# Kernel tuning notes

Hardware: AMD Instinct MI355X
Metric: run time of the kernel (lower is better)

## Reference

```python
import jax, jax.numpy as jnp
import numpy as np

D = 1024
B, T = 4, 2048


def _ln(x, g, b, eps=1e-5):
    mu = jnp.mean(x, axis=-1, keepdims=True)
    var = jnp.mean((x - mu) ** 2, axis=-1, keepdims=True)
    return (x - mu) * jax.lax.rsqrt(var + eps) * g + b


def setup_inputs() -> dict:
    key = jax.random.key(0)
    ks = jax.random.split(key, 24)
    s = 0.02
    lin = lambda k, o, i: jax.random.normal(k, (o, i), jnp.float32) * s
    return {
        "x": jax.random.normal(ks[0], (B, T, D), jnp.float32),
        "g1": jnp.ones((D,), jnp.float32),
        "be1": jnp.zeros((D,), jnp.float32),
        "w_lin1": lin(ks[1], D, D), "b_lin1": jnp.zeros((D,), jnp.float32),
        "wq": lin(ks[2], D, D), "bq": jnp.zeros((D,), jnp.float32),
        "wk": lin(ks[3], D, D), "bk": jnp.zeros((D,), jnp.float32),
        "wv": lin(ks[4], D, D), "bv": jnp.zeros((D,), jnp.float32),
        "w_lin2": lin(ks[5], D, D), "b_lin2": jnp.zeros((D,), jnp.float32),
        "g2": jnp.ones((D,), jnp.float32),
        "be2": jnp.zeros((D,), jnp.float32),
        "w_ff1": lin(ks[6], 2 * D, D), "b_ff1": jnp.zeros((2 * D,), jnp.float32),
        "w_ff2": lin(ks[7], D, 2 * D), "b_ff2": jnp.zeros((D,), jnp.float32),
    }


def reference(x, g1, be1, w_lin1, b_lin1, wq, bq, wk, bk, wv, bv,
              w_lin2, b_lin2, g2, be2, w_ff1, b_ff1, w_ff2, b_ff2):
    # x: [B,T,D]. Torch Linear: y = x @ W.T + b with W: [out,in]
    x = _ln(x, g1, be1)
    x = x @ w_lin1.T + b_lin1
    # single-head self-attention, scale = 1/sqrt(d_model) (matches source)
    q = x @ wq.T + bq
    k = x @ wk.T + bk
    v = x @ wv.T + bv
    scores = jnp.einsum('btd,bsd->bts', q, k) / jnp.sqrt(jnp.float32(x.shape[-1]))
    mask = jnp.tril(jnp.ones((x.shape[1], x.shape[1]), bool))  # [T,T]
    scores = jnp.where(mask, scores, -jnp.inf)
    probs = jax.nn.softmax(scores, axis=-1)
    attn = jnp.einsum('bts,bsd->btd', probs, v)
    x = x + (attn @ w_lin2.T + b_lin2)
    # FFN on norm2(x), exact (erf) GELU as torch default
    h = _ln(x, g2, be2)
    h = jax.nn.gelu(h @ w_ff1.T + b_ff1, approximate=False)
    x = x + (h @ w_ff2.T + b_ff2)
    return x
```

## Files before the change

kernel.cpp:

```cpp
#include <hip/hip_runtime.h>

typedef __attribute__((ext_vector_type(4))) float f32x4;
typedef __attribute__((ext_vector_type(8))) short short8;
typedef __attribute__((ext_vector_type(4))) unsigned short u16x4;
typedef __attribute__((ext_vector_type(8))) unsigned short u16x8;

#define MFMA(a, b, c) __builtin_amdgcn_mfma_f32_16x16x32_bf16(a, b, c, 0, 0, 0)
#define GLOAD16(g, l) __builtin_amdgcn_global_load_lds( \
    (const __attribute__((address_space(1))) unsigned int*)(g), \
    (__attribute__((address_space(3))) unsigned int*)(l), 16, 0, 0)

#define BARX() __builtin_amdgcn_s_barrier()
#define LGK0() asm volatile("s_waitcnt lgkmcnt(0)" ::: "memory")
#define VM6 asm volatile("s_waitcnt vmcnt(6)" ::: "memory")
#define VM0 asm volatile("s_waitcnt vmcnt(0)" ::: "memory")
#define NOWAIT ((void)0)

__device__ inline unsigned short f2bf(float f) {
    unsigned int u = __float_as_uint(f);
    u += 0x7fffu + ((u >> 16) & 1u);
    return (unsigned short)(u >> 16);
}

__global__ __launch_bounds__(256) void cvt_kernel(const float* __restrict__ in,
                                                  unsigned short* __restrict__ out, int n4) {
    int i = blockIdx.x * 256 + threadIdx.x;
    if (i < n4) {
        f32x4 v = *(const f32x4*)(in + (long long)i * 4);
        u16x4 o;
#pragma unroll
        for (int j = 0; j < 4; j++) o[j] = f2bf(v[j]);
        *(u16x4*)&out[(long long)i * 4] = o;
    }
}

__global__ __launch_bounds__(256) void ln_kernel(const float* __restrict__ x,
                                                 const float* __restrict__ g,
                                                 const float* __restrict__ be,
                                                 unsigned short* __restrict__ out) {
    const int row = blockIdx.x, tid = threadIdx.x;
    const float* px = x + (long long)row * 1024;
    f32x4 v = *(const f32x4*)(px + tid * 4);
    float s = v[0] + v[1] + v[2] + v[3];
    float q = v[0] * v[0] + v[1] * v[1] + v[2] * v[2] + v[3] * v[3];
#pragma unroll
    for (int o = 32; o; o >>= 1) { s += __shfl_xor(s, o); q += __shfl_xor(q, o); }
    __shared__ float sm[10];
    const int lane = tid & 63, wid = tid >> 6;
    if (lane == 0) { sm[wid] = s; sm[4 + wid] = q; }
    __syncthreads();
    if (tid == 0) {
        float ts = sm[0] + sm[1] + sm[2] + sm[3];
        float tq = sm[4] + sm[5] + sm[6] + sm[7];
        float mean = ts * (1.f / 1024.f);
        float var = tq * (1.f / 1024.f) - mean * mean;
        sm[8] = mean; sm[9] = rsqrtf(var + 1e-5f);
    }
    __syncthreads();
    float mean = sm[8], rs = sm[9];
    f32x4 gg = *(const f32x4*)(g + tid * 4);
    f32x4 bb = *(const f32x4*)(be + tid * 4);
    u16x4 o;
#pragma unroll
    for (int i = 0; i < 4; i++) o[i] = f2bf((v[i] - mean) * rs * gg[i] + bb[i]);
    *(u16x4*)&out[(long long)row * 1024 + tid * 4] = o;
}

__global__ __launch_bounds__(256) void softmax_kernel(float* __restrict__ S) {
    const int T = 2048;
    const int t = blockIdx.x, b = blockIdx.y, tid = threadIdx.x;
    float* row = S + ((long long)b * T + t) * T;
    const int base = tid * 8;
    f32x4 v0 = *(const f32x4*)(row + base);
    f32x4 v1 = *(const f32x4*)(row + base + 4);
    float mx = -1e30f;
#pragma unroll
    for (int i = 0; i < 4; i++) {
        if (base + i <= t)     mx = fmaxf(mx, v0[i]);
        if (base + 4 + i <= t) mx = fmaxf(mx, v1[i]);
    }
#pragma unroll
    for (int o = 32; o; o >>= 1) mx = fmaxf(mx, __shfl_xor(mx, o));
    __shared__ float sm[10];
    const int lane = tid & 63, wid = tid >> 6;
    if (lane == 0) sm[wid] = mx;
    __syncthreads();
    if (tid == 0) sm[8] = fmaxf(fmaxf(sm[0], sm[1]), fmaxf(sm[2], sm[3]));
    __syncthreads();
    float M = sm[8];
    float e[8]; float s = 0.f;
#pragma unroll
    for (int i = 0; i < 4; i++) {
        e[i]     = (base + i <= t)     ? __expf(v0[i] - M) : 0.f;
        e[4 + i] = (base + 4 + i <= t) ? __expf(v1[i] - M) : 0.f;
        s += e[i] + e[4 + i];
    }
#pragma unroll
    for (int o = 32; o; o >>= 1) s += __shfl_xor(s, o);
    if (lane == 0) sm[4 + wid] = s;
    __syncthreads();
    if (tid == 0) sm[9] = 1.f / (sm[4] + sm[5] + sm[6] + sm[7]);
    __syncthreads();
    float inv = sm[9];
    unsigned short* P = (unsigned short*)row;
    u16x8 o;
#pragma unroll
    for (int i = 0; i < 8; i++) o[i] = f2bf(e[i] * inv);
    *(u16x8*)&P[base] = o;
}

#define TILE(CB, PB, KPRE, PF, WAITER) do {                                         \
    const unsigned short* Lc = LDS + (CB) * 24576;                                  \
    unsigned short* Lp = LDS + (PB) * 24576;                                        \
    short8 Af0, Af1, Af2, Af3, Bf[4];                                               \
    Af0 = *(const short8*)(Lc + ao[0] + ks0);                                       \
    Af1 = *(const short8*)(Lc + ao[1] + ks0);                                       \
    _Pragma("unroll") for (int j = 0; j < 4; j++)                                   \
        Bf[j] = *(const short8*)(Lc + bo[j] + ks0);                                 \
    if (PF) { GLOAD16(srcA[0] + (KPRE), Lp + dstA[0]);                              \
              GLOAD16(srcA[1] + (KPRE), Lp + dstA[1]);                              \
              GLOAD16(srcA[2] + (KPRE), Lp + dstA[2]); }                            \
    BARX(); LGK0();                                                                 \
    __builtin_amdgcn_s_setprio(1);                                                  \
    _Pragma("unroll") for (int j = 0; j < 4; j++) {                                 \
        acc[0][j] = MFMA(Af0, Bf[j], acc[0][j]);                                    \
        acc[1][j] = MFMA(Af1, Bf[j], acc[1][j]); }                                  \
    __builtin_amdgcn_s_setprio(0); BARX();                                          \
    Af2 = *(const short8*)(Lc + ao[2] + ks0);                                       \
    Af3 = *(const short8*)(Lc + ao[3] + ks0);                                       \
    if (PF) { GLOAD16(srcA[3] + (KPRE), Lp + dstA[3]);                              \
              GLOAD16(srcB[0] + (KPRE), Lp + dstB[0]);                              \
              GLOAD16(srcB[1] + (KPRE), Lp + dstB[1]); }                            \
    BARX(); LGK0();                                                                 \
    __builtin_amdgcn_s_setprio(1);                                                  \
    _Pragma("unroll") for (int j = 0; j < 4; j++) {                                 \
        acc[2][j] = MFMA(Af2, Bf[j], acc[2][j]);                                    \
        acc[3][j] = MFMA(Af3, Bf[j], acc[3][j]); }                                  \
    __builtin_amdgcn_s_setprio(0); BARX();                                          \
    Af0 = *(const short8*)(Lc + ao[0] + ks1);                                       \
    Af1 = *(const short8*)(Lc + ao[1] + ks1);                                       \
    _Pragma("unroll") for (int j = 0; j < 4; j++)                                   \
        Bf[j] = *(const short8*)(Lc + bo[j] + ks1);                                 \
    BARX(); LGK0();                                                                 \
    __builtin_amdgcn_s_setprio(1);                                                  \
    _Pragma("unroll") for (int j = 0; j < 4; j++) {                                 \
        acc[0][j] = MFMA(Af0, Bf[j], acc[0][j]);                                    \
        acc[1][j] = MFMA(Af1, Bf[j], acc[1][j]); }                                  \
    __builtin_amdgcn_s_setprio(0); BARX();                                          \
    Af2 = *(const short8*)(Lc + ao[2] + ks1);                                       \
    Af3 = *(const short8*)(Lc + ao[3] + ks1);                                       \
    WAITER;                                                                         \
    BARX(); LGK0();                                                                 \
    __builtin_amdgcn_s_setprio(1);                                                  \
    _Pragma("unroll") for (int j = 0; j < 4; j++) {                                 \
        acc[2][j] = MFMA(Af2, Bf[j], acc[2][j]);                                    \
        acc[3][j] = MFMA(Af3, Bf[j], acc[3][j]); }                                  \
    __builtin_amdgcn_s_setprio(0); BARX();                                          \
} while (0)

template <int MODE>
__global__ __launch_bounds__(512, 2) void gemm_bt(
    const unsigned short* __restrict__ A, int lda, long long sA,
    const unsigned short* __restrict__ Bw, int ldb, long long sB,
    const float* __restrict__ bias,
    const float* __restrict__ resid, long long sR,
    float* __restrict__ outf, unsigned short* __restrict__ outb,
    int ldo, long long sO, int K, float scale, int flags) {
    const int m0 = blockIdx.y * 256, n0 = blockIdx.x * 128;
    if ((flags & 1) && n0 >= m0 + 256) return;
    const int bz = blockIdx.z;
    A += (long long)bz * sA; Bw += (long long)bz * sB;
    if (resid) resid += (long long)bz * sR;
    if (outf) outf += (long long)bz * sO;
    if (outb) outb += (long long)bz * sO;
    const int Keff = (flags & 2) ? (m0 + 256 < K ? m0 + 256 : K) : K;
    const int nt = Keff >> 6;

    __shared__ __align__(16) unsigned short LDS[3 * 24576];

    const int tid = threadIdx.x, lane = tid & 63, wid = tid >> 6;

    const unsigned short* srcA[4]; int dstA[4];
    const unsigned short* srcB[2]; int dstB[2];
#pragma unroll
    for (int g = 0; g < 4; g++) {
        int p = g * 512 + wid * 64 + lane;
        int r = p >> 3, cs = (p & 7) ^ (r & 7);
        srcA[g] = A + (long long)(m0 + r) * lda + cs * 8;
        dstA[g] = g * 4096 + wid * 512;
    }
#pragma unroll
    for (int g = 0; g < 2; g++) {
        int p = g * 512 + wid * 64 + lane;
        int r = p >> 3, cs = (p & 7) ^ (r & 7);
        srcB[g] = Bw + (long long)(n0 + r) * ldb + cs * 8;
        dstB[g] = 16384 + g * 4096 + wid * 512;
    }

    const int wm = (wid >> 1) * 64, wn = (wid & 1) * 64;
    const int fr = lane & 15;
    int ao[4], bo[4];
#pragma unroll
    for (int i = 0; i < 4; i++) ao[i] = (wm + i * 16 + fr) * 64;
#pragma unroll
    for (int j = 0; j < 4; j++) bo[j] = 16384 + (wn + j * 16 + fr) * 64;
    const int ks0 = (((lane >> 4)) ^ (fr & 7)) * 8;
    const int ks1 = ((4 + (lane >> 4)) ^ (fr & 7)) * 8;

    f32x4 acc[4][4] = {};

#pragma unroll
    for (int g = 0; g < 4; g++) GLOAD16(srcA[g], LDS + dstA[g]);
#pragma unroll
    for (int g = 0; g < 2; g++) GLOAD16(srcB[g], LDS + dstB[g]);
#pragma unroll
    for (int g = 0; g < 4; g++) GLOAD16(srcA[g] + 64, LDS + 24576 + dstA[g]);
#pragma unroll
    for (int g = 0; g < 2; g++) GLOAD16(srcB[g] + 64, LDS + 24576 + dstB[g]);
    VM6; BARX();
    __builtin_amdgcn_sched_barrier(0);

    int c = 0, p = 2, kpre = 128;
    for (int t = 0; t < nt - 2; ++t) {
        TILE(c, p, kpre, true, VM6);
        c = (c == 2) ? 0 : c + 1;
        p = (p == 2) ? 0 : p + 1;
        kpre += 64;
    }
    TILE(c, p, 0, false, VM0);
    c = (c == 2) ? 0 : c + 1;
    TILE(c, p, 0, false, NOWAIT);

    const int cc = lane & 15, rr = (lane >> 4) * 4;
#pragma unroll
    for (int fm = 0; fm < 4; fm++)
#pragma unroll
        for (int fn = 0; fn < 4; fn++) {
            f32x4 av = acc[fm][fn];
            int colg = n0 + wn + fn * 16 + cc;
            int rowg0 = m0 + wm + fm * 16 + rr;
            float bv = bias ? bias[colg] : 0.f;
            if (MODE == 3) {
                u16x4 o;
#pragma unroll
                for (int i = 0; i < 4; i++) o[i] = f2bf((av[i] + bv) * scale);
                *(u16x4*)&outb[(long long)colg * ldo + rowg0] = o;
            } else {
#pragma unroll
                for (int i = 0; i < 4; i++) {
                    float v = av[i] + bv;
                    long long idx = (long long)(rowg0 + i) * ldo + colg;
                    if (MODE == 0) outf[idx] = v;
                    if (MODE == 1) outf[idx] = v + resid[idx];
                    if (MODE == 2) outb[idx] = f2bf(v * scale);
                    if (MODE == 4) { outf[idx] = v; outb[idx] = f2bf(v); }
                    if (MODE == 5) outb[idx] = f2bf(0.5f * v * (1.f + erff(v * 0.70710678f)));
                }
            }
        }
}

extern "C" void kernel_launch(void* const* d_in, const int* in_sizes, int n_in,
                              void* d_out, int out_size, void* d_ws, size_t ws_size,
                              hipStream_t stream) {
    const float* x      = (const float*)d_in[0];
    const float* g1     = (const float*)d_in[1];
    const float* be1    = (const float*)d_in[2];
    const float* b_lin1 = (const float*)d_in[4];
    const float* bq     = (const float*)d_in[6];
    const float* bk     = (const float*)d_in[8];
    const float* bv     = (const float*)d_in[10];
    const float* b_lin2 = (const float*)d_in[12];
    const float* g2     = (const float*)d_in[13];
    const float* be2    = (const float*)d_in[14];
    const float* b_ff1  = (const float*)d_in[16];
    const float* b_ff2  = (const float*)d_in[18];

    const long long MB = 1024LL * 1024LL;
    char* ws = (char*)d_ws;
    unsigned short* xn1 = (unsigned short*)(ws + 0);
    unsigned short* x1b = (unsigned short*)(ws + 16 * MB);
    float*          S   = (float*)(ws + 0);
    float*          x1f = (float*)(ws + 64 * MB);
    unsigned short* xn2 = (unsigned short*)(ws + 64 * MB);
    unsigned short* qb  = (unsigned short*)(ws + 96 * MB);
    unsigned short* kb  = (unsigned short*)(ws + 112 * MB);
    unsigned short* vT  = (unsigned short*)(ws + 128 * MB);
    unsigned short* attn= (unsigned short*)(ws + 96 * MB);
    unsigned short* h   = (unsigned short*)(ws + 96 * MB);
    float*          x2  = (float*)(ws + 144 * MB);
    unsigned short* wb1 = (unsigned short*)(ws + 176 * MB);
    unsigned short* wbq = (unsigned short*)(ws + 178 * MB);
    unsigned short* wbk = (unsigned short*)(ws + 180 * MB);
    unsigned short* wbv = (unsigned short*)(ws + 182 * MB);
    unsigned short* wb2 = (unsigned short*)(ws + 184 * MB);
    unsigned short* wbf1= (unsigned short*)(ws + 186 * MB);
    unsigned short* wbf2= (unsigned short*)(ws + 190 * MB);

    auto cvt = [&](const void* src, unsigned short* dst, long long n) {
        int n4 = (int)(n / 4);
        cvt_kernel<<<(n4 + 255) / 256, 256, 0, stream>>>((const float*)src, dst, n4);
    };
    cvt(d_in[3], wb1, 1048576);
    cvt(d_in[5], wbq, 1048576);
    cvt(d_in[7], wbk, 1048576);
    cvt(d_in[9], wbv, 1048576);
    cvt(d_in[11], wb2, 1048576);
    cvt(d_in[15], wbf1, 2097152);
    cvt(d_in[17], wbf2, 2097152);

    ln_kernel<<<8192, 256, 0, stream>>>(x, g1, be1, xn1);
    gemm_bt<4><<<dim3(8, 32, 1), 512, 0, stream>>>(xn1, 1024, 0, wb1, 1024, 0, b_lin1,
        nullptr, 0, x1f, x1b, 1024, 0, 1024, 1.f, 0);
    gemm_bt<2><<<dim3(8, 32, 1), 512, 0, stream>>>(x1b, 1024, 0, wbq, 1024, 0, bq,
        nullptr, 0, nullptr, qb, 1024, 0, 1024, 0.03125f, 0);
    gemm_bt<2><<<dim3(8, 32, 1), 512, 0, stream>>>(x1b, 1024, 0, wbk, 1024, 0, bk,
        nullptr, 0, nullptr, kb, 1024, 0, 1024, 1.f, 0);
    gemm_bt<3><<<dim3(8, 8, 4), 512, 0, stream>>>(x1b, 1024, 2048LL * 1024, wbv, 1024, 0, bv,
        nullptr, 0, nullptr, vT, 2048, 2097152LL, 1024, 1.f, 0);
    gemm_bt<0><<<dim3(16, 8, 4), 512, 0, stream>>>(qb, 1024, 2097152LL, kb, 1024, 2097152LL,
        nullptr, nullptr, 0, S, nullptr, 2048, 4194304LL, 1024, 1.f, 1);
    softmax_kernel<<<dim3(2048, 4), 256, 0, stream>>>(S);
    gemm_bt<2><<<dim3(8, 8, 4), 512, 0, stream>>>((unsigned short*)S, 4096, 8388608LL,
        vT, 2048, 2097152LL, nullptr, nullptr, 0, nullptr, attn, 1024, 2097152LL, 2048, 1.f, 2);
    gemm_bt<1><<<dim3(8, 32, 1), 512, 0, stream>>>(attn, 1024, 0, wb2, 1024, 0, b_lin2,
        x1f, 0, x2, nullptr, 1024, 0, 1024, 1.f, 0);
    ln_kernel<<<8192, 256, 0, stream>>>(x2, g2, be2, xn2);
    gemm_bt<5><<<dim3(16, 32, 1), 512, 0, stream>>>(xn2, 1024, 0, wbf1, 1024, 0, b_ff1,
        nullptr, 0, nullptr, h, 2048, 0, 1024, 1.f, 0);
    gemm_bt<1><<<dim3(8, 32, 1), 512, 0, stream>>>(h, 2048, 0, wbf2, 2048, 0, b_ff2,
        x2, 0, (float*)d_out, nullptr, 1024, 0, 2048, 1.f, 0);
}
```

Baseline: 512.8 us.

## Add 256x256-tile GEMM, fuse Q/K projections, fold Q scale into weights

Adds a gemm_wide kernel with 256x256 output tiles and a K-step of 32 (8x4 fragments per wave), used for the fused QK projection, the QK^T scores and the FF1 GEMM. Q and K projections become one GEMM over contiguous wbq/wbk weights with a concatenated bias, and the 1/32 attention scale is folded into the Q weight conversion and bias. The existing tile macro is restructured to issue all four A fragments per MFMA group, halving barrier phases. Larger tiles cut global reloads and launches, but raise register pressure and leave fewer blocks for the grid.

```diff
diff --git a/kernel.cpp b/kernel.cpp
--- a/kernel.cpp
+++ b/kernel.cpp
@@ -13,6 +13,7 @@
 #define BARX() __builtin_amdgcn_s_barrier()
 #define LGK0() asm volatile("s_waitcnt lgkmcnt(0)" ::: "memory")
 #define VM6 asm volatile("s_waitcnt vmcnt(6)" ::: "memory")
+#define VM4 asm volatile("s_waitcnt vmcnt(4)" ::: "memory")
 #define VM0 asm volatile("s_waitcnt vmcnt(0)" ::: "memory")
 #define NOWAIT ((void)0)
 
@@ -23,15 +24,24 @@
 }
 
 __global__ __launch_bounds__(256) void cvt_kernel(const float* __restrict__ in,
-                                                  unsigned short* __restrict__ out, int n4) {
+                                                  unsigned short* __restrict__ out, int n4,
+                                                  float scale) {
     int i = blockIdx.x * 256 + threadIdx.x;
     if (i < n4) {
         f32x4 v = *(const f32x4*)(in + (long long)i * 4);
         u16x4 o;
 #pragma unroll
-        for (int j = 0; j < 4; j++) o[j] = f2bf(v[j]);
+        for (int j = 0; j < 4; j++) o[j] = f2bf(v[j] * scale);
         *(u16x4*)&out[(long long)i * 4] = o;
     }
+}
+
+__global__ __launch_bounds__(256) void biascat_kernel(const float* __restrict__ bq,
+                                                      const float* __restrict__ bk,
+                                                      float* __restrict__ out) {
+    int i = blockIdx.x * 256 + threadIdx.x;
+    if (i < 1024) out[i] = bq[i] * 0.03125f;
+    else if (i < 2048) out[i] = bk[i - 1024];
 }
 
 __global__ __launch_bounds__(256) void ln_kernel(const float* __restrict__ x,
@@ -109,12 +119,42 @@
     *(u16x8*)&P[base] = o;
 }
 
-#define TILE(CB, PB, KPRE, PF, WAITER) do {                                         \
+#define EPILOGUE(FM_COUNT) do {                                                     \
+    const int cc = lane & 15, rr = (lane >> 4) * 4;                                 \
+    _Pragma("unroll")                                                               \
+    for (int fm = 0; fm < FM_COUNT; fm++)                                           \
+        _Pragma("unroll")                                                           \
+        for (int fn = 0; fn < 4; fn++) {                                            \
+            f32x4 av = acc[fm][fn];                                                 \
+            int colg = n0 + wn + fn * 16 + cc;                                      \
+            int rowg0 = m0 + wm + fm * 16 + rr;                                     \
+            float bv = bias ? bias[colg] : 0.f;                                     \
+            if (MODE == 3) {                                                        \
+                u16x4 o;                                                            \
+                _Pragma("unroll")                                                   \
+                for (int i = 0; i < 4; i++) o[i] = f2bf((av[i] + bv) * scale);      \
+                *(u16x4*)&outb[(long long)colg * ldo + rowg0] = o;                  \
+            } else {                                                                \
+                _Pragma("unroll")                                                   \
+                for (int i = 0; i < 4; i++) {                                       \
+                    float v = av[i] + bv;                                           \
+                    long long idx = (long long)(rowg0 + i) * ldo + colg;            \
+                    if (MODE == 0) outf[idx] = v;                                   \
+                    if (MODE == 1) outf[idx] = v + resid[idx];                      \
+                    if (MODE == 2) outb[idx] = f2bf(v * scale);                     \
+                    if (MODE == 4) { outf[idx] = v; outb[idx] = f2bf(v); }          \
+                    if (MODE == 5) outb[idx] = f2bf(0.5f * v * (1.f + erff(v * 0.70710678f))); \
+                }                                                                   \
+            }                                                                       \
+        }                                                                           \
+} while (0)
+
+#define TILE_B(CB, PB, KPRE, PF, WAITER) do {                                       \
     const unsigned short* Lc = LDS + (CB) * 24576;                                  \
     unsigned short* Lp = LDS + (PB) * 24576;                                        \
-    short8 Af0, Af1, Af2, Af3, Bf[4];                                               \
-    Af0 = *(const short8*)(Lc + ao[0] + ks0);                                       \
-    Af1 = *(const short8*)(Lc + ao[1] + ks0);                                       \
+    short8 Af[4], Bf[4];                                                            \
+    _Pragma("unroll") for (int i = 0; i < 4; i++)                                   \
+        Af[i] = *(const short8*)(Lc + ao[i] + ks0);                                 \
     _Pragma("unroll") for (int j = 0; j < 4; j++)                                   \
         Bf[j] = *(const short8*)(Lc + bo[j] + ks0);                                 \
     if (PF) { GLOAD16(srcA[0] + (KPRE), Lp + dstA[0]);                              \
@@ -122,39 +162,23 @@
               GLOAD16(srcA[2] + (KPRE), Lp + dstA[2]); }                            \
     BARX(); LGK0();                                                                 \
     __builtin_amdgcn_s_setprio(1);                                                  \
-    _Pragma("unroll") for (int j = 0; j < 4; j++) {                                 \
-        acc[0][j] = MFMA(Af0, Bf[j], acc[0][j]);                                    \
-        acc[1][j] = MFMA(Af1, Bf[j], acc[1][j]); }                                  \
+    _Pragma("unroll") for (int i = 0; i < 4; i++)                                   \
+        _Pragma("unroll") for (int j = 0; j < 4; j++)                               \
+            acc[i][j] = MFMA(Af[i], Bf[j], acc[i][j]);                              \
     __builtin_amdgcn_s_setprio(0); BARX();                                          \
-    Af2 = *(const short8*)(Lc + ao[2] + ks0);                                       \
-    Af3 = *(const short8*)(Lc + ao[3] + ks0);                                       \
+    _Pragma("unroll") for (int i = 0; i < 4; i++)                                   \
+        Af[i] = *(const short8*)(Lc + ao[i] + ks1);                                 \
+    _Pragma("unroll") for (int j = 0; j < 4; j++)                                   \
+        Bf[j] = *(const short8*)(Lc + bo[j] + ks1);                                 \
     if (PF) { GLOAD16(srcA[3] + (KPRE), Lp + dstA[3]);                              \
               GLOAD16(srcB[0] + (KPRE), Lp + dstB[0]);                              \
               GLOAD16(srcB[1] + (KPRE), Lp + dstB[1]); }                            \
-    BARX(); LGK0();                                                                 \
-    __builtin_amdgcn_s_setprio(1);                                                  \
-    _Pragma("unroll") for (int j = 0; j < 4; j++) {                                 \
-        acc[2][j] = MFMA(Af2, Bf[j], acc[2][j]);                                    \
-        acc[3][j] = MFMA(Af3, Bf[j], acc[3][j]); }                                  \
-    __builtin_amdgcn_s_setprio(0); BARX();                                          \
-    Af0 = *(const short8*)(Lc + ao[0] + ks1);                                       \
-    Af1 = *(const short8*)(Lc + ao[1] + ks1);                                       \
-    _Pragma("unroll") for (int j = 0; j < 4; j++)                                   \
-        Bf[j] = *(const short8*)(Lc + bo[j] + ks1);                                 \
-    BARX(); LGK0();                                                                 \
-    __builtin_amdgcn_s_setprio(1);                                                  \
-    _Pragma("unroll") for (int j = 0; j < 4; j++) {                                 \
-        acc[0][j] = MFMA(Af0, Bf[j], acc[0][j]);                                    \
-        acc[1][j] = MFMA(Af1, Bf[j], acc[1][j]); }                                  \
-    __builtin_amdgcn_s_setprio(0); BARX();                                          \
-    Af2 = *(const short8*)(Lc + ao[2] + ks1);                                       \
-    Af3 = *(const short8*)(Lc + ao[3] + ks1);                                       \
     WAITER;                                                                         \
     BARX(); LGK0();                                                                 \
     __builtin_amdgcn_s_setprio(1);                                                  \
-    _Pragma("unroll") for (int j = 0; j < 4; j++) {                                 \
-        acc[2][j] = MFMA(Af2, Bf[j], acc[2][j]);                                    \
-        acc[3][j] = MFMA(Af3, Bf[j], acc[3][j]); }                                  \
+    _Pragma("unroll") for (int i = 0; i < 4; i++)                                   \
+        _Pragma("unroll") for (int j = 0; j < 4; j++)                               \
+            acc[i][j] = MFMA(Af[i], Bf[j], acc[i][j]);                              \
     __builtin_amdgcn_s_setprio(0); BARX();                                          \
 } while (0)
 
@@ -222,42 +246,112 @@
 
     int c = 0, p = 2, kpre = 128;
     for (int t = 0; t < nt - 2; ++t) {
-        TILE(c, p, kpre, true, VM6);
+        TILE_B(c, p, kpre, true, VM6);
         c = (c == 2) ? 0 : c + 1;
         p = (p == 2) ? 0 : p + 1;
         kpre += 64;
     }
-    TILE(c, p, 0, false, VM0);
+    TILE_B(c, p, 0, false, VM0);
     c = (c == 2) ? 0 : c + 1;
-    TILE(c, p, 0, false, NOWAIT);
-
-    const int cc = lane & 15, rr = (lane >> 4) * 4;
-#pragma unroll
-    for (int fm = 0; fm < 4; fm++)
-#pragma unroll
-        for (int fn = 0; fn < 4; fn++) {
-            f32x4 av = acc[fm][fn];
-            int colg = n0 + wn + fn * 16 + cc;
-            int rowg0 = m0 + wm + fm * 16 + rr;
-            float bv = bias ? bias[colg] : 0.f;
-            if (MODE == 3) {
-                u16x4 o;
-#pragma unroll
-                for (int i = 0; i < 4; i++) o[i] = f2bf((av[i] + bv) * scale);
-                *(u16x4*)&outb[(long long)colg * ldo + rowg0] = o;
-            } else {
-#pragma unroll
-                for (int i = 0; i < 4; i++) {
-                    float v = av[i] + bv;
-                    long long idx = (long long)(rowg0 + i) * ldo + colg;
-                    if (MODE == 0) outf[idx] = v;
-                    if (MODE == 1) outf[idx] = v + resid[idx];
-                    if (MODE == 2) outb[idx] = f2bf(v * scale);
-                    if (MODE == 4) { outf[idx] = v; outb[idx] = f2bf(v); }
-                    if (MODE == 5) outb[idx] = f2bf(0.5f * v * (1.f + erff(v * 0.70710678f)));
-                }
-            }
-        }
+    TILE_B(c, p, 0, false, NOWAIT);
+
+    EPILOGUE(4);
+}
+
+#define TILE_A(CB, PB, KPRE, PF, WAITER) do {                                       \
+    const unsigned short* Lc = LDS + (CB) * 16384;                                  \
+    unsigned short* Lp = LDS + (PB) * 16384;                                        \
+    short8 Af[4], Bf[4];                                                            \
+    _Pragma("unroll") for (int i = 0; i < 4; i++)                                   \
+        Af[i] = *(const short8*)(Lc + aoW[i] + ksW);                                \
+    _Pragma("unroll") for (int j = 0; j < 4; j++)                                   \
+        Bf[j] = *(const short8*)(Lc + boW[j] + ksW);                                \
+    if (PF) { GLOAD16(srcA[0] + (KPRE), Lp + dstA[0]);                              \
+              GLOAD16(srcB[0] + (KPRE), Lp + dstB[0]); }                            \
+    BARX(); LGK0();                                                                 \
+    __builtin_amdgcn_s_setprio(1);                                                  \
+    _Pragma("unroll") for (int i = 0; i < 4; i++)                                   \
+        _Pragma("unroll") for (int j = 0; j < 4; j++)                               \
+            acc[i][j] = MFMA(Af[i], Bf[j], acc[i][j]);                              \
+    __builtin_amdgcn_s_setprio(0); BARX();                                          \
+    _Pragma("unroll") for (int i = 0; i < 4; i++)                                   \
+        Af[i] = *(const short8*)(Lc + aoW[4 + i] + ksW);                            \
+    if (PF) { GLOAD16(srcA[1] + (KPRE), Lp + dstA[1]);                              \
+              GLOAD16(srcB[1] + (KPRE), Lp + dstB[1]); }                            \
+    WAITER;                                                                         \
+    BARX(); LGK0();                                                                 \
+    __builtin_amdgcn_s_setprio(1);                                                  \
+    _Pragma("unroll") for (int i = 0; i < 4; i++)                                   \
+        _Pragma("unroll") for (int j = 0; j < 4; j++)                               \
+            acc[4 + i][j] = MFMA(Af[i], Bf[j], acc[4 + i][j]);                      \
+    __builtin_amdgcn_s_setprio(0); BARX();                                          \
+} while (0)
+
+template <int MODE>
+__global__ __launch_bounds__(512, 2) void gemm_wide(
+    const unsigned short* __restrict__ A, int lda, long long sA,
+    const unsigned short* __restrict__ Bw, int ldb, long long sB,
+    const float* __restrict__ bias,
+    const float* __restrict__ resid, long long sR,
+    float* __restrict__ outf, unsigned short* __restrict__ outb,
+    int ldo, long long sO, int K, float scale, int flags) {
+    const int m0 = blockIdx.y * 256, n0 = blockIdx.x * 256;
+    if ((flags & 1) && n0 > m0) return;
+    const int bz = blockIdx.z;
+    A += (long long)bz * sA; Bw += (long long)bz * sB;
+    if (resid) resid += (long long)bz * sR;
+    if (outf) outf += (long long)bz * sO;
+    if (outb) outb += (long long)bz * sO;
+    const int nt = K >> 5;
+
+    __shared__ __align__(16) unsigned short LDS[3 * 16384];
+
+    const int tid = threadIdx.x, lane = tid & 63, wid = tid >> 6;
+
+    const unsigned short* srcA[2]; int dstA[2];
+    const unsigned short* srcB[2]; int dstB[2];
+#pragma unroll
+    for (int g = 0; g < 2; g++) {
+        int p = g * 512 + wid * 64 + lane;
+        int r = p >> 2, cs = (p & 3) ^ ((r >> 1) & 3);
+        srcA[g] = A + (long long)(m0 + r) * lda + cs * 8;
+        dstA[g] = g * 4096 + wid * 512;
+        srcB[g] = Bw + (long long)(n0 + r) * ldb + cs * 8;
+        dstB[g] = 8192 + g * 4096 + wid * 512;
+    }
+
+    const int wm = (wid >> 2) * 128, wn = (wid & 3) * 64;
+    const int fr = lane & 15;
+    int aoW[8], boW[4];
+#pragma unroll
+    for (int i = 0; i < 8; i++) aoW[i] = (wm + i * 16 + fr) * 32;
+#pragma unroll
+    for (int j = 0; j < 4; j++) boW[j] = 8192 + (wn + j * 16 + fr) * 32;
+    const int ksW = ((lane >> 4) ^ ((fr >> 1) & 3)) * 8;
+
+    f32x4 acc[8][4] = {};
+
+#pragma unroll
+    for (int g = 0; g < 2; g++) { GLOAD16(srcA[g], LDS + dstA[g]);
+                                  GLOAD16(srcB[g], LDS + dstB[g]); }
+#pragma unroll
+    for (int g = 0; g < 2; g++) { GLOAD16(srcA[g] + 32, LDS + 16384 + dstA[g]);
+                                  GLOAD16(srcB[g] + 32, LDS + 16384 + dstB[g]); }
+    VM4; BARX();
+    __builtin_amdgcn_sched_barrier(0);
+
+    int c = 0, p = 2, kpre = 64;
+    for (int t = 0; t < nt - 2; ++t) {
+        TILE_A(c, p, kpre, true, VM4);
+        c = (c == 2) ? 0 : c + 1;
+        p = (p == 2) ? 0 : p + 1;
+        kpre += 32;
+    }
+    TILE_A(c, p, 0, false, VM0);
+    c = (c == 2) ? 0 : c + 1;
+    TILE_A(c, p, 0, false, NOWAIT);
+
+    EPILOGUE(8);
 }
 
 extern "C" void kernel_launch(void* const* d_in, const int* in_sizes, int n_in,
@@ -281,10 +375,10 @@
     unsigned short* xn1 = (unsigned short*)(ws + 0);
     unsigned short* x1b = (unsigned short*)(ws + 16 * MB);
     float*          S   = (float*)(ws + 0);
+    float*          bqk = (float*)(ws + 60 * MB);
     float*          x1f = (float*)(ws + 64 * MB);
     unsigned short* xn2 = (unsigned short*)(ws + 64 * MB);
-    unsigned short* qb  = (unsigned short*)(ws + 96 * MB);
-    unsigned short* kb  = (unsigned short*)(ws + 112 * MB);
+    unsigned short* qk  = (unsigned short*)(ws + 96 * MB);
     unsigned short* vT  = (unsigned short*)(ws + 128 * MB);
     unsigned short* attn= (unsigned short*)(ws + 96 * MB);
     unsigned short* h   = (unsigned short*)(ws + 96 * MB);
@@ -297,28 +391,27 @@
     unsigned short* wbf1= (unsigned short*)(ws + 186 * MB);
     unsigned short* wbf2= (unsigned short*)(ws + 190 * MB);
 
-    auto cvt = [&](const void* src, unsigned short* dst, long long n) {
+    auto cvt = [&](const void* src, unsigned short* dst, long long n, float sc) {
         int n4 = (int)(n / 4);
-        cvt_kernel<<<(n4 + 255) / 256, 256, 0, stream>>>((const float*)src, dst, n4);
+        cvt_kernel<<<(n4 + 255) / 256, 256, 0, stream>>>((const float*)src, dst, n4, sc);
     };
-    cvt(d_in[3], wb1, 1048576);
-    cvt(d_in[5], wbq, 1048576);
-    cvt(d_in[7], wbk, 1048576);
-    cvt(d_in[9], wbv, 1048576);
-    cvt(d_in[11], wb2, 1048576);
-    cvt(d_in[15], wbf1, 2097152);
-    cvt(d_in[17], wbf2, 2097152);
+    cvt(d_in[3], wb1, 1048576, 1.f);
+    cvt(d_in[5], wbq, 1048576, 0.03125f);
+    cvt(d_in[7], wbk, 1048576, 1.f);
+    cvt(d_in[9], wbv, 1048576, 1.f);
+    cvt(d_in[11], wb2, 1048576, 1.f);
+    cvt(d_in[15], wbf1, 2097152, 1.f);
+    cvt(d_in[17], wbf2, 2097152, 1.f);
+    biascat_kernel<<<8, 256, 0, stream>>>(bq, bk, bqk);
 
     ln_kernel<<<8192, 256, 0, stream>>>(x, g1, be1, xn1);
     gemm_bt<4><<<dim3(8, 32, 1), 512, 0, stream>>>(xn1, 1024, 0, wb1, 1024, 0, b_lin1,
         nullptr, 0, x1f, x1b, 1024, 0, 1024, 1.f, 0);
-    gemm_bt<2><<<dim3(8, 32, 1), 512, 0, stream>>>(x1b, 1024, 0, wbq, 1024, 0, bq,
-        nullptr, 0, nullptr, qb, 1024, 0, 1024, 0.03125f, 0);
-    gemm_bt<2><<<dim3(8, 32, 1), 512, 0, stream>>>(x1b, 1024, 0, wbk, 1024, 0, bk,
-        nullptr, 0, nullptr, kb, 1024, 0, 1024, 1.f, 0);
+    gemm_wide<2><<<dim3(8, 32, 1), 512, 0, stream>>>(x1b, 1024, 0, wbq, 1024, 0, bqk,
+        nullptr, 0, nullptr, qk, 2048, 0, 1024, 1.f, 0);
     gemm_bt<3><<<dim3(8, 8, 4), 512, 0, stream>>>(x1b, 1024, 2048LL * 1024, wbv, 1024, 0, bv,
         nullptr, 0, nullptr, vT, 2048, 2097152LL, 1024, 1.f, 0);
-    gemm_bt<0><<<dim3(16, 8, 4), 512, 0, stream>>>(qb, 1024, 2097152LL, kb, 1024, 2097152LL,
+    gemm_wide<0><<<dim3(8, 8, 4), 512, 0, stream>>>(qk, 2048, 4194304LL, qk + 1024, 2048, 4194304LL,
         nullptr, nullptr, 0, S, nullptr, 2048, 4194304LL, 1024, 1.f, 1);
     softmax_kernel<<<dim3(2048, 4), 256, 0, stream>>>(S);
     gemm_bt<2><<<dim3(8, 8, 4), 512, 0, stream>>>((unsigned short*)S, 4096, 8388608LL,
@@ -326,7 +419,7 @@
     gemm_bt<1><<<dim3(8, 32, 1), 512, 0, stream>>>(attn, 1024, 0, wb2, 1024, 0, b_lin2,
         x1f, 0, x2, nullptr, 1024, 0, 1024, 1.f, 0);
     ln_kernel<<<8192, 256, 0, stream>>>(x2, g2, be2, xn2);
-    gemm_bt<5><<<dim3(16, 32, 1), 512, 0, stream>>>(xn2, 1024, 0, wbf1, 1024, 0, b_ff1,
+    gemm_wide<5><<<dim3(8, 32, 1), 512, 0, stream>>>(xn2, 1024, 0, wbf1, 1024, 0, b_ff1,
         nullptr, 0, nullptr, h, 2048, 0, 1024, 1.f, 0);
     gemm_bt<1><<<dim3(8, 32, 1), 512, 0, stream>>>(h, 2048, 0, wbf2, 2048, 0, b_ff2,
         x2, 0, (float*)d_out, nullptr, 1024, 0, 2048, 1.f, 0);
```

Result: faster. 494.6 us (-3.5%).
